# Kernel optimization log

Measured on AMD Instinct MI355X. Metric: run time of the kernel, lower is better.

## Reference

```python
import jax, jax.numpy as jnp
import numpy as np

T, N = 32, 256
HID, NL = 64, 1
D_CH, Hg, Wg = 2, 8, 8            # obs shape (2, 8, 8); d must be 2 to match Conv2d(2*HID, 2*HID)
NSUB, SUBDIM = 6, 3               # subtasks shape (n_subtasks, subtask_dim)
OBS_V, SUB_V, NACT = 16, 20, 6    # vocab sizes; action_space.n = NSUB
OBS_LEN = D_CH * Hg * Wg          # 128
SUB_LEN = NSUB * SUBDIM           # 18
GRU_IN = HID * (OBS_LEN + SUBDIM) # 8384
STATE = 2 + NL * HID + NACT + NSUB  # a(1)+v(1)+h(64)+a_probs(6)+p(6) = 78


def setup_inputs() -> dict:
    key = jax.random.key(0)
    ks = jax.random.split(key, 12)
    obs_idx = jax.random.randint(ks[0], (T, N, OBS_LEN), 0, OBS_V)
    sub_idx = jax.random.randint(ks[1], (T, N, SUB_LEN), 0, SUB_V)
    act = jax.random.randint(ks[2], (T, N, 1), 0, NACT)  # all >= 0 -> sample_new is a no-op
    inputs = jnp.concatenate([obs_idx, sub_idx, act], -1).astype(jnp.float32)
    hx = jnp.zeros((1, N, STATE), jnp.float32)  # all-zero -> new_episode everywhere
    sd = lambda f: 1.0 / np.sqrt(f)
    return dict(
        inputs=inputs,
        hx=hx,
        subtask_emb=jax.random.normal(ks[3], (SUB_V, HID)),
        obs_emb=jax.random.normal(ks[4], (OBS_V, HID)),
        conv_w=jax.random.normal(ks[5], (2 * HID, 2 * HID)) * sd(2 * HID),
        conv_b=jnp.zeros((2 * HID,)),
        w_ih=jax.random.normal(ks[6], (3 * HID, GRU_IN)) * sd(GRU_IN),
        w_hh=jax.random.normal(ks[7], (3 * HID, HID)) * sd(HID),
        b_ih=jnp.zeros((3 * HID,)),
        b_hh=jnp.zeros((3 * HID,)),
        critic_w=jax.random.normal(ks[8], (1, HID)) * sd(HID),
        critic_b=jnp.zeros((1,)),
        phi_w=jax.random.normal(ks[9], (1, HID)) * sd(HID),
        phi_b=jnp.zeros((1,)),
    )


def _forward(inputs, hx, subtask_emb, obs_emb, conv_w, conv_b, w_ih, w_hh,
             b_ih, b_hh, critic_w, critic_b, phi_w, phi_b):
    ints = inputs.astype(jnp.int32)
    obs_all = ints[:, :, :OBS_LEN]                      # (T,N,128)
    sub_all = ints[:, :, OBS_LEN:OBS_LEN + SUB_LEN]     # (T,N,18)
    act_all = ints[:, :, -1]                            # (T,N)

    # subtask memory from first timestep: (N, NSUB, SUBDIM*HID)
    M = subtask_emb[sub_all[0]].reshape(N, NSUB, SUBDIM * HID)

    hx0 = hx[0]
    new_episode = jnp.all(hx0 == 0, axis=-1)            # (N,)
    # recurrent state split order a(1), v(1), h(NL*HID), a_probs(NACT), p(NSUB)
    h0 = hx0[:, 2:2 + NL * HID].reshape(N, NL, HID).transpose(1, 0, 2)  # (NL,N,HID)
    p0 = hx0[:, 2 + NL * HID + NACT:]
    p0 = p0.at[:, 0].set(jnp.where(new_episode, 1.0, p0[:, 0]))

    def gru_cell(x, h):
        gx = x @ w_ih.T + b_ih
        gh = h @ w_hh.T + b_hh
        r = jax.nn.sigmoid(gx[:, :HID] + gh[:, :HID])
        z = jax.nn.sigmoid(gx[:, HID:2 * HID] + gh[:, HID:2 * HID])
        n = jnp.tanh(gx[:, 2 * HID:] + r * gh[:, 2 * HID:])
        return (1 - z) * n + z * h

    def step(carry, xt):
        h, p = carry
        obs_t, act_t = xt
        r_vec = jnp.einsum('ns,nsk->nk', p, M)          # (p.unsqueeze(1) @ M).squeeze(1)
        emb = obs_emb[obs_t.reshape(N, D_CH, Hg, Wg)]   # (N,2,H,W,HID)
        conv_in = emb.transpose(0, 1, 4, 2, 3).reshape(N, 2 * HID, Hg * Wg)
        conv_out = jnp.einsum('ncp,oc->nop', conv_in, conv_w) + conv_b[None, :, None]  # 1x1 conv
        gru_in = jnp.concatenate([conv_out.reshape(N, -1), r_vec], -1)
        hn = gru_cell(gru_in, h[0])                     # single-layer GRU, seq len 1
        h_new = hn[None]
        c = jax.nn.sigmoid(hn @ phi_w.T + phi_b)        # (N,1)
        # torch.roll(F.pad(p,(0,1)), 1) flattened: pad column is 0, so this is a
        # right-shift with 0 fill; p1[:, -1] == p[:, -1].
        p1 = jnp.concatenate([jnp.zeros((N, 1), p.dtype), p[:, :-1]], axis=1)
        p2 = p1 + p * p[:, -1:]
        p_new = (1 - c) * p + c * p2
        probs = p_new / p_new.sum(-1, keepdims=True)    # FixedCategorical(p).probs
        v = hn @ critic_w.T + critic_b                  # (N,1)
        a = act_t.astype(jnp.float32)[:, None]          # actions all >=0 -> no resampling
        h_flat = h_new.transpose(1, 0, 2).reshape(N, -1)
        ys = jnp.concatenate([a, v, h_flat, probs, p_new], -1)
        return (h_new, p_new), ys

    _, hx_out = jax.lax.scan(step, (h0, p0), (obs_all, act_all))  # (T,N,78)
    return hx_out


def reference(inputs, hx, subtask_emb, obs_emb, conv_w, conv_b, w_ih, w_hh,
              b_ih, b_hh, critic_w, critic_b, phi_w, phi_b):
    hx_out = _forward(inputs, hx, subtask_emb, obs_emb, conv_w, conv_b, w_ih,
                      w_hh, b_ih, b_hh, critic_w, critic_b, phi_w, phi_b)
    return (hx_out, hx_out[-1:])
```

## Files before the change

### kernel.cpp

```cpp
#include <hip/hip_runtime.h>
#include <hip/hip_bf16.h>
#include <math.h>

#define TT 32
#define NN 256
#define HID 64
#define OBS_LEN 128
#define SUB_LEN 18
#define IN_ROW 147
#define GJ 192
#define GRU_IN 8384
#define STATE 78
#define NSUB 6

__device__ __forceinline__ float sigm(float x) {
    return 1.0f / (1.0f + __expf(-x));
}

__device__ __forceinline__ unsigned short f2bf(float f) {
    unsigned u = __float_as_uint(f);
    u += 0x7fffu + ((u >> 16) & 1u);
    return (unsigned short)(u >> 16);
}

__global__ void k_T(const float* __restrict__ w_ih, float* __restrict__ wT) {
    __shared__ float tile[32][33];
    int i0 = blockIdx.x * 32;
    int j0 = blockIdx.y * 32;
    int tx = threadIdx.x, ty = threadIdx.y;
    for (int a = ty; a < 32; a += 8)
        tile[a][tx] = w_ih[(size_t)(j0 + a) * GRU_IN + i0 + tx];
    __syncthreads();
    for (int a = ty; a < 32; a += 8)
        wT[(size_t)(i0 + a) * GJ + j0 + tx] = tile[tx][a];
}

__global__ void k_G(const float* __restrict__ obs_emb, const float* __restrict__ conv_w,
                    float* __restrict__ G) {
    int i = blockIdx.x * blockDim.x + threadIdx.x;
    if (i >= 128 * 2 * 16) return;
    int v = i & 15, d = (i >> 4) & 1, o = i >> 5;
    float acc = 0.f;
    const float* oe = obs_emb + v * 64;
    const float* cw = conv_w + o * 128 + d * 64;
    #pragma unroll
    for (int hd = 0; hd < 64; hd++) acc = fmaf(oe[hd], cw[hd], acc);
    G[i] = acc;
}

__global__ void k_CB(const float* __restrict__ conv_b, const float* __restrict__ w_ih,
                     const float* __restrict__ b_ih, float* __restrict__ CB2) {
    int j = blockIdx.x;
    int tid = threadIdx.x;
    const float* wr = w_ih + (size_t)j * GRU_IN;
    float acc = 0.f;
    for (int i = tid; i < 8192; i += 256) acc = fmaf(conv_b[i >> 6], wr[i], acc);
    __shared__ float red[4];
    for (int off = 32; off > 0; off >>= 1) acc += __shfl_down(acc, off, 64);
    if ((tid & 63) == 0) red[tid >> 6] = acc;
    __syncthreads();
    if (tid == 0) CB2[j] = b_ih[j] + red[0] + red[1] + red[2] + red[3];
}

__global__ __launch_bounds__(192) void k_Q(const float* __restrict__ inputs,
                                           const float* __restrict__ subtask_emb,
                                           const float* __restrict__ wT,
                                           float* __restrict__ Q) {
    int n = blockIdx.x;
    int j = threadIdx.x;
    __shared__ int sidx[SUB_LEN];
    __shared__ __align__(16) float Ms[GJ * 8];
    if (j < SUB_LEN) sidx[j] = (int)inputs[(size_t)n * IN_ROW + OBS_LEN + j];
    __syncthreads();
    for (int e = j; e < NSUB * GJ; e += GJ) {
        int s = e / GJ, k = e - s * GJ;
        int row = sidx[s * 3 + (k >> 6)];
        Ms[k * 8 + s] = subtask_emb[row * 64 + (k & 63)];
    }
    __syncthreads();
    float acc[NSUB] = {0.f, 0.f, 0.f, 0.f, 0.f, 0.f};
    const float* base = wT + (size_t)8192 * GJ + j;
    for (int k = 0; k < GJ; k++) {
        float w = base[(size_t)k * GJ];
        float4 m0 = *(const float4*)&Ms[k * 8];
        float2 m1 = *(const float2*)&Ms[k * 8 + 4];
        acc[0] = fmaf(m0.x, w, acc[0]);
        acc[1] = fmaf(m0.y, w, acc[1]);
        acc[2] = fmaf(m0.z, w, acc[2]);
        acc[3] = fmaf(m0.w, w, acc[3]);
        acc[4] = fmaf(m1.x, w, acc[4]);
        acc[5] = fmaf(m1.y, w, acc[5]);
    }
    for (int s = 0; s < NSUB; s++) Q[((size_t)n * NSUB + s) * GJ + j] = acc[s];
}

__global__ __launch_bounds__(192) void k_E(const float* __restrict__ G,
                                           const float* __restrict__ wT,
                                           unsigned short* __restrict__ E16) {
    int bp = blockIdx.x;
    int dp = bp >> 1, half = bp & 1;
    int d = dp >> 6, p = dp & 63;
    int j = threadIdx.x;
    __shared__ __align__(16) float Gs[128 * 8];
    for (int e = j; e < 1024; e += GJ) {
        int o = e >> 3, vv = e & 7;
        Gs[e] = G[(o << 5) + (d << 4) + (half << 3) + vv];
    }
    __syncthreads();
    float acc[8];
    #pragma unroll
    for (int v = 0; v < 8; v++) acc[v] = 0.f;
    const float* wb = wT + (size_t)p * GJ + j;
    for (int o = 0; o < 128; o++) {
        float w = wb[(size_t)(o * 64) * GJ];
        float4 g0 = *(const float4*)&Gs[o * 8];
        float4 g1 = *(const float4*)&Gs[o * 8 + 4];
        acc[0] = fmaf(g0.x, w, acc[0]);
        acc[1] = fmaf(g0.y, w, acc[1]);
        acc[2] = fmaf(g0.z, w, acc[2]);
        acc[3] = fmaf(g0.w, w, acc[3]);
        acc[4] = fmaf(g1.x, w, acc[4]);
        acc[5] = fmaf(g1.y, w, acc[5]);
        acc[6] = fmaf(g1.z, w, acc[6]);
        acc[7] = fmaf(g1.w, w, acc[7]);
    }
    unsigned short* Eo = E16 + ((size_t)(dp * 16 + half * 8)) * GJ;
    #pragma unroll
    for (int v = 0; v < 8; v++) Eo[v * GJ + j] = f2bf(acc[v]);
}

__global__ __launch_bounds__(192) void k_gx(const float* __restrict__ inputs,
                                            const unsigned short* __restrict__ E16,
                                            const float* __restrict__ CB2,
                                            float* __restrict__ gx_all) {
    int tn0 = blockIdx.x * 2;
    int tid = threadIdx.x;
    int g = tid / 96;
    int jj = (tid - g * 96) * 2;
    int tn = tn0 + g;
    __shared__ int idx[2][OBS_LEN];
    for (int e = tid; e < 2 * OBS_LEN; e += 192)
        idx[e >> 7][e & 127] = (int)inputs[(size_t)(tn0 + (e >> 7)) * IN_ROW + (e & 127)];
    __syncthreads();
    float a0 = CB2[jj], a1 = CB2[jj + 1];
    const int* id = idx[g];
    #pragma unroll 8
    for (int dp = 0; dp < OBS_LEN; dp++) {
        unsigned u = *(const unsigned*)(E16 + ((size_t)(dp * 16 + id[dp])) * GJ + jj);
        a0 += __uint_as_float(u << 16);
        a1 += __uint_as_float(u & 0xffff0000u);
    }
    float2 r; r.x = a0; r.y = a1;
    *(float2*)(gx_all + (size_t)tn * GJ + jj) = r;
}

__global__ __launch_bounds__(192) void k_rec(const float* __restrict__ inputs,
                                             const float* __restrict__ hx,
                                             const float* __restrict__ w_hh,
                                             const float* __restrict__ b_hh,
                                             const float* __restrict__ critic_w,
                                             const float* __restrict__ critic_b,
                                             const float* __restrict__ phi_w,
                                             const float* __restrict__ phi_b,
                                             const float* __restrict__ Q,
                                             const float* __restrict__ gx_all,
                                             float* __restrict__ out) {
    int n = blockIdx.x;
    int tid = threadIdx.x;

    __shared__ __align__(16) float gx_lds[TT * GJ];
    __shared__ __align__(16) float h_sh[64];
    __shared__ __align__(16) float p_sh[8];
    __shared__ float sum_sh[GJ];
    __shared__ float ghn_sh[64];
    __shared__ float act_sh[TT];
    __shared__ float sc;
    __shared__ int nz_cnt;

    for (int e = tid * 4; e < TT * GJ; e += 192 * 4) {
        int t = e / GJ, j = e - t * GJ;
        float4 v = *(const float4*)(gx_all + ((size_t)t * NN + n) * GJ + j);
        *(float4*)&gx_lds[e] = v;
    }
    if (tid < TT)
        act_sh[tid] = inputs[((size_t)tid * NN + n) * IN_ROW + (IN_ROW - 1)];

    float wreg[64];
    {
        const float4* wr = (const float4*)(w_hh + (size_t)tid * 64);
        #pragma unroll
        for (int h4 = 0; h4 < 16; h4++) {
            float4 w = wr[h4];
            wreg[h4 * 4 + 0] = w.x;
            wreg[h4 * 4 + 1] = w.y;
            wreg[h4 * 4 + 2] = w.z;
            wreg[h4 * 4 + 3] = w.w;
        }
    }
    float q[NSUB];
    #pragma unroll
    for (int s = 0; s < NSUB; s++) q[s] = Q[((size_t)n * NSUB + s) * GJ + tid];
    float bhh = b_hh[tid];
    float pw = (tid < 64) ? phi_w[tid] : 0.f;
    float cw = (tid < 64) ? critic_w[tid] : 0.f;
    float phib = phi_b[0], crtb = critic_b[0];

    if (tid == 0) nz_cnt = 0;
    __syncthreads();
    if (tid < STATE) {
        float hv = hx[(size_t)n * STATE + tid];
        if (hv != 0.f) atomicAdd(&nz_cnt, 1);
        if (tid >= 2 && tid < 66) h_sh[tid - 2] = hv;
        if (tid >= 72) p_sh[tid - 72] = hv;
    }
    __syncthreads();
    if (tid == 0 && nz_cnt == 0) p_sh[0] = 1.0f;
    __syncthreads();

    for (int t = 0; t < TT; t++) {
        float4 pv = *(const float4*)&p_sh[0];
        float2 pv2 = *(const float2*)&p_sh[4];
        float gx = gx_lds[t * GJ + tid];
        gx = fmaf(pv.x, q[0], gx);
        gx = fmaf(pv.y, q[1], gx);
        gx = fmaf(pv.z, q[2], gx);
        gx = fmaf(pv.w, q[3], gx);
        gx = fmaf(pv2.x, q[4], gx);
        gx = fmaf(pv2.y, q[5], gx);
        float a0 = 0.f, a1 = 0.f, a2 = 0.f, a3 = 0.f;
        #pragma unroll
        for (int h = 0; h < 64; h += 8) {
            float4 ha = *(const float4*)&h_sh[h];
            float4 hb = *(const float4*)&h_sh[h + 4];
            a0 = fmaf(ha.x, wreg[h + 0], a0);
            a1 = fmaf(ha.y, wreg[h + 1], a1);
            a2 = fmaf(ha.z, wreg[h + 2], a2);
            a3 = fmaf(ha.w, wreg[h + 3], a3);
            a0 = fmaf(hb.x, wreg[h + 4], a0);
            a1 = fmaf(hb.y, wreg[h + 5], a1);
            a2 = fmaf(hb.z, wreg[h + 6], a2);
            a3 = fmaf(hb.w, wreg[h + 7], a3);
        }
        float gh = bhh + ((a0 + a1) + (a2 + a3));
        sum_sh[tid] = (tid < 128) ? (gx + gh) : gx;
        if (tid >= 128) ghn_sh[tid - 128] = gh;
        __syncthreads();

        if (tid < 64) {
            float r = sigm(sum_sh[tid]);
            float z = sigm(sum_sh[64 + tid]);
            float x2 = fmaf(r, ghn_sh[tid], sum_sh[128 + tid]);
            float e2 = __expf(2.f * x2);
            float nv = 1.f - 2.f / (e2 + 1.f);
            float hold = h_sh[tid];
            float hn = fmaf(z, hold - nv, nv);
            float pc = hn * pw, vc = hn * cw;
            #pragma unroll
            for (int off = 32; off > 0; off >>= 1) {
                pc += __shfl_down(pc, off, 64);
                vc += __shfl_down(vc, off, 64);
            }
            pc = __shfl(pc, 0, 64);
            float c = sigm(pc + phib);
            if (tid == 0) sc = vc + crtb;
            h_sh[tid] = hn;
            if (tid < NSUB) {
                float pold = p_sh[tid];
                float pm1 = (tid > 0) ? p_sh[tid - 1] : 0.f;
                float p5 = p_sh[5];
                float p2 = pm1 + pold * p5;
                float pn = (1.f - c) * pold + c * p2;
                p_sh[tid] = pn;
            }
        }
        __syncthreads();

        if (tid < STATE) {
            float val;
            if (tid == 0) val = act_sh[t];
            else if (tid == 1) val = sc;
            else if (tid < 66) val = h_sh[tid - 2];
            else if (tid < 72) {
                float ps = p_sh[0] + p_sh[1] + p_sh[2] + p_sh[3] + p_sh[4] + p_sh[5];
                val = p_sh[tid - 66] / ps;
            } else val = p_sh[tid - 72];
            size_t base = ((size_t)t * NN + n) * STATE;
            out[base + tid] = val;
            if (t == TT - 1)
                out[(size_t)TT * NN * STATE + (size_t)n * STATE + tid] = val;
        }
    }
}

extern "C" void kernel_launch(void* const* d_in, const int* in_sizes, int n_in,
                              void* d_out, int out_size, void* d_ws, size_t ws_size,
                              hipStream_t stream) {
    const float* inputs      = (const float*)d_in[0];
    const float* hx          = (const float*)d_in[1];
    const float* subtask_emb = (const float*)d_in[2];
    const float* obs_emb     = (const float*)d_in[3];
    const float* conv_w      = (const float*)d_in[4];
    const float* conv_b      = (const float*)d_in[5];
    const float* w_ih        = (const float*)d_in[6];
    const float* w_hh        = (const float*)d_in[7];
    const float* b_ih        = (const float*)d_in[8];
    const float* b_hh        = (const float*)d_in[9];
    const float* critic_w    = (const float*)d_in[10];
    const float* critic_b    = (const float*)d_in[11];
    const float* phi_w       = (const float*)d_in[12];
    const float* phi_b       = (const float*)d_in[13];
    float* out = (float*)d_out;

    float* ws   = (float*)d_ws;
    float* wT   = ws;
    float* G    = wT + (size_t)GRU_IN * GJ;
    float* CB2  = G + 4096;
    float* Ef   = CB2 + 192;
    unsigned short* E16 = (unsigned short*)Ef;
    float* Q    = Ef + 196608;
    float* gx   = Q + (size_t)NN * NSUB * GJ;

    k_T<<<dim3(GRU_IN / 32, GJ / 32), dim3(32, 8), 0, stream>>>(w_ih, wT);
    k_G<<<16, 256, 0, stream>>>(obs_emb, conv_w, G);
    k_CB<<<GJ, 256, 0, stream>>>(conv_b, w_ih, b_ih, CB2);
    k_Q<<<NN, GJ, 0, stream>>>(inputs, subtask_emb, wT, Q);
    k_E<<<256, GJ, 0, stream>>>(G, wT, E16);
    k_gx<<<TT * NN / 2, GJ, 0, stream>>>(inputs, E16, CB2, gx);
    k_rec<<<NN, GJ, 0, stream>>>(inputs, hx, w_hh, b_hh, critic_w, critic_b,
                                 phi_w, phi_b, Q, gx, out);
}
```

Baseline: 193.7 us.

## Merge setup kernels and run GRU recurrence in a single wavefront per sequence

Three independent preprocessing kernels (weight transpose, conv-embedding table, bias fold) are merged into one launch, and the E and Q precompute kernels into another, cutting launch count from seven to four. The recurrent kernel now uses one 64-lane wavefront per batch element: each lane holds three rows of w_hh in registers and computes all three gates for its hidden unit. This removes the per-step __syncthreads and shared-memory exchange of gate sums, and keeps p in registers with the reductions done by xor shuffles. The trade-off is a much higher register load per lane (192 weight floats) and only 256 single-wave blocks, which lowers occupancy and could cause spills.

```diff
diff --git a/kernel.cpp b/kernel.cpp
--- a/kernel.cpp
+++ b/kernel.cpp
@@ -12,6 +12,7 @@
 #define GRU_IN 8384
 #define STATE 78
 #define NSUB 6
+#define NT_TILES 1572
 
 __device__ __forceinline__ float sigm(float x) {
     return 1.0f / (1.0f + __expf(-x));
@@ -23,110 +24,123 @@
     return (unsigned short)(u >> 16);
 }
 
-__global__ void k_T(const float* __restrict__ w_ih, float* __restrict__ wT) {
+__device__ __forceinline__ float2 pkfma(float2 a, float2 b, float2 c) {
+    float2 r;
+    r.x = fmaf(a.x, b.x, c.x);
+    r.y = fmaf(a.y, b.y, c.y);
+    return r;
+}
+
+__global__ __launch_bounds__(256) void k_TGC(const float* __restrict__ w_ih,
+                                             const float* __restrict__ obs_emb,
+                                             const float* __restrict__ conv_w,
+                                             const float* __restrict__ conv_b,
+                                             const float* __restrict__ b_ih,
+                                             float* __restrict__ wT,
+                                             float* __restrict__ G,
+                                             float* __restrict__ CB2) {
+    int b = blockIdx.x;
+    int tid = threadIdx.x;
     __shared__ float tile[32][33];
-    int i0 = blockIdx.x * 32;
-    int j0 = blockIdx.y * 32;
-    int tx = threadIdx.x, ty = threadIdx.y;
-    for (int a = ty; a < 32; a += 8)
-        tile[a][tx] = w_ih[(size_t)(j0 + a) * GRU_IN + i0 + tx];
-    __syncthreads();
-    for (int a = ty; a < 32; a += 8)
-        wT[(size_t)(i0 + a) * GJ + j0 + tx] = tile[tx][a];
-}
-
-__global__ void k_G(const float* __restrict__ obs_emb, const float* __restrict__ conv_w,
-                    float* __restrict__ G) {
-    int i = blockIdx.x * blockDim.x + threadIdx.x;
-    if (i >= 128 * 2 * 16) return;
-    int v = i & 15, d = (i >> 4) & 1, o = i >> 5;
-    float acc = 0.f;
-    const float* oe = obs_emb + v * 64;
-    const float* cw = conv_w + o * 128 + d * 64;
-    #pragma unroll
-    for (int hd = 0; hd < 64; hd++) acc = fmaf(oe[hd], cw[hd], acc);
-    G[i] = acc;
-}
-
-__global__ void k_CB(const float* __restrict__ conv_b, const float* __restrict__ w_ih,
-                     const float* __restrict__ b_ih, float* __restrict__ CB2) {
-    int j = blockIdx.x;
-    int tid = threadIdx.x;
-    const float* wr = w_ih + (size_t)j * GRU_IN;
-    float acc = 0.f;
-    for (int i = tid; i < 8192; i += 256) acc = fmaf(conv_b[i >> 6], wr[i], acc);
     __shared__ float red[4];
-    for (int off = 32; off > 0; off >>= 1) acc += __shfl_down(acc, off, 64);
-    if ((tid & 63) == 0) red[tid >> 6] = acc;
-    __syncthreads();
-    if (tid == 0) CB2[j] = b_ih[j] + red[0] + red[1] + red[2] + red[3];
-}
-
-__global__ __launch_bounds__(192) void k_Q(const float* __restrict__ inputs,
-                                           const float* __restrict__ subtask_emb,
-                                           const float* __restrict__ wT,
-                                           float* __restrict__ Q) {
-    int n = blockIdx.x;
+
+    if (b < NT_TILES) {
+        int bx = b % 262, by = b / 262;
+        int i0 = bx * 32, j0 = by * 32;
+        int tx = tid & 31, ty = tid >> 5;
+        for (int a = ty; a < 32; a += 8)
+            tile[a][tx] = w_ih[(size_t)(j0 + a) * GRU_IN + i0 + tx];
+        __syncthreads();
+        for (int a = ty; a < 32; a += 8)
+            wT[(size_t)(i0 + a) * GJ + j0 + tx] = tile[tx][a];
+    } else if (b < NT_TILES + 16) {
+        int i = (b - NT_TILES) * 256 + tid;
+        int v = i & 15, d = (i >> 4) & 1, o = i >> 5;
+        float acc = 0.f;
+        const float* oe = obs_emb + v * 64;
+        const float* cw = conv_w + o * 128 + d * 64;
+        #pragma unroll
+        for (int hd = 0; hd < 64; hd++) acc = fmaf(oe[hd], cw[hd], acc);
+        G[i] = acc;
+    } else {
+        int j = b - (NT_TILES + 16);
+        const float* wr = w_ih + (size_t)j * GRU_IN;
+        float acc = 0.f;
+        for (int i = tid; i < 8192; i += 256) acc = fmaf(conv_b[i >> 6], wr[i], acc);
+        for (int off = 32; off > 0; off >>= 1) acc += __shfl_down(acc, off, 64);
+        if ((tid & 63) == 0) red[tid >> 6] = acc;
+        __syncthreads();
+        if (tid == 0) CB2[j] = b_ih[j] + red[0] + red[1] + red[2] + red[3];
+    }
+}
+
+__global__ __launch_bounds__(192) void k_EQ(const float* __restrict__ inputs,
+                                            const float* __restrict__ subtask_emb,
+                                            const float* __restrict__ G,
+                                            const float* __restrict__ wT,
+                                            unsigned short* __restrict__ E16,
+                                            float* __restrict__ Q) {
+    int b = blockIdx.x;
     int j = threadIdx.x;
-    __shared__ int sidx[SUB_LEN];
-    __shared__ __align__(16) float Ms[GJ * 8];
-    if (j < SUB_LEN) sidx[j] = (int)inputs[(size_t)n * IN_ROW + OBS_LEN + j];
-    __syncthreads();
-    for (int e = j; e < NSUB * GJ; e += GJ) {
-        int s = e / GJ, k = e - s * GJ;
-        int row = sidx[s * 3 + (k >> 6)];
-        Ms[k * 8 + s] = subtask_emb[row * 64 + (k & 63)];
-    }
-    __syncthreads();
-    float acc[NSUB] = {0.f, 0.f, 0.f, 0.f, 0.f, 0.f};
-    const float* base = wT + (size_t)8192 * GJ + j;
-    for (int k = 0; k < GJ; k++) {
-        float w = base[(size_t)k * GJ];
-        float4 m0 = *(const float4*)&Ms[k * 8];
-        float2 m1 = *(const float2*)&Ms[k * 8 + 4];
-        acc[0] = fmaf(m0.x, w, acc[0]);
-        acc[1] = fmaf(m0.y, w, acc[1]);
-        acc[2] = fmaf(m0.z, w, acc[2]);
-        acc[3] = fmaf(m0.w, w, acc[3]);
-        acc[4] = fmaf(m1.x, w, acc[4]);
-        acc[5] = fmaf(m1.y, w, acc[5]);
-    }
-    for (int s = 0; s < NSUB; s++) Q[((size_t)n * NSUB + s) * GJ + j] = acc[s];
-}
-
-__global__ __launch_bounds__(192) void k_E(const float* __restrict__ G,
-                                           const float* __restrict__ wT,
-                                           unsigned short* __restrict__ E16) {
-    int bp = blockIdx.x;
-    int dp = bp >> 1, half = bp & 1;
-    int d = dp >> 6, p = dp & 63;
-    int j = threadIdx.x;
-    __shared__ __align__(16) float Gs[128 * 8];
-    for (int e = j; e < 1024; e += GJ) {
-        int o = e >> 3, vv = e & 7;
-        Gs[e] = G[(o << 5) + (d << 4) + (half << 3) + vv];
-    }
-    __syncthreads();
-    float acc[8];
-    #pragma unroll
-    for (int v = 0; v < 8; v++) acc[v] = 0.f;
-    const float* wb = wT + (size_t)p * GJ + j;
-    for (int o = 0; o < 128; o++) {
-        float w = wb[(size_t)(o * 64) * GJ];
-        float4 g0 = *(const float4*)&Gs[o * 8];
-        float4 g1 = *(const float4*)&Gs[o * 8 + 4];
-        acc[0] = fmaf(g0.x, w, acc[0]);
-        acc[1] = fmaf(g0.y, w, acc[1]);
-        acc[2] = fmaf(g0.z, w, acc[2]);
-        acc[3] = fmaf(g0.w, w, acc[3]);
-        acc[4] = fmaf(g1.x, w, acc[4]);
-        acc[5] = fmaf(g1.y, w, acc[5]);
-        acc[6] = fmaf(g1.z, w, acc[6]);
-        acc[7] = fmaf(g1.w, w, acc[7]);
-    }
-    unsigned short* Eo = E16 + ((size_t)(dp * 16 + half * 8)) * GJ;
-    #pragma unroll
-    for (int v = 0; v < 8; v++) Eo[v * GJ + j] = f2bf(acc[v]);
+
+    if (b < 256) {
+        int dp = b >> 1, half = b & 1;
+        int d = dp >> 6, p = dp & 63;
+        __shared__ __align__(16) float Gs[128 * 8];
+        for (int e = j; e < 1024; e += GJ) {
+            int o = e >> 3, vv = e & 7;
+            Gs[e] = G[(o << 5) + (d << 4) + (half << 3) + vv];
+        }
+        __syncthreads();
+        float acc[8];
+        #pragma unroll
+        for (int v = 0; v < 8; v++) acc[v] = 0.f;
+        const float* wb = wT + (size_t)p * GJ + j;
+        #pragma unroll 4
+        for (int o = 0; o < 128; o++) {
+            float w = wb[(size_t)(o * 64) * GJ];
+            float4 g0 = *(const float4*)&Gs[o * 8];
+            float4 g1 = *(const float4*)&Gs[o * 8 + 4];
+            acc[0] = fmaf(g0.x, w, acc[0]);
+            acc[1] = fmaf(g0.y, w, acc[1]);
+            acc[2] = fmaf(g0.z, w, acc[2]);
+            acc[3] = fmaf(g0.w, w, acc[3]);
+            acc[4] = fmaf(g1.x, w, acc[4]);
+            acc[5] = fmaf(g1.y, w, acc[5]);
+            acc[6] = fmaf(g1.z, w, acc[6]);
+            acc[7] = fmaf(g1.w, w, acc[7]);
+        }
+        unsigned short* Eo = E16 + ((size_t)(dp * 16 + half * 8)) * GJ;
+        #pragma unroll
+        for (int v = 0; v < 8; v++) Eo[v * GJ + j] = f2bf(acc[v]);
+    } else {
+        int n = b - 256;
+        __shared__ int sidx[SUB_LEN];
+        __shared__ __align__(16) float Ms[GJ * 8];
+        if (j < SUB_LEN) sidx[j] = (int)inputs[(size_t)n * IN_ROW + OBS_LEN + j];
+        __syncthreads();
+        for (int e = j; e < NSUB * GJ; e += GJ) {
+            int s = e / GJ, k = e - s * GJ;
+            int row = sidx[s * 3 + (k >> 6)];
+            Ms[k * 8 + s] = subtask_emb[row * 64 + (k & 63)];
+        }
+        __syncthreads();
+        float acc[NSUB] = {0.f, 0.f, 0.f, 0.f, 0.f, 0.f};
+        const float* base = wT + (size_t)8192 * GJ + j;
+        #pragma unroll 4
+        for (int k = 0; k < GJ; k++) {
+            float w = base[(size_t)k * GJ];
+            float4 m0 = *(const float4*)&Ms[k * 8];
+            float2 m1 = *(const float2*)&Ms[k * 8 + 4];
+            acc[0] = fmaf(m0.x, w, acc[0]);
+            acc[1] = fmaf(m0.y, w, acc[1]);
+            acc[2] = fmaf(m0.z, w, acc[2]);
+            acc[3] = fmaf(m0.w, w, acc[3]);
+            acc[4] = fmaf(m1.x, w, acc[4]);
+            acc[5] = fmaf(m1.y, w, acc[5]);
+        }
+        for (int s = 0; s < NSUB; s++) Q[((size_t)n * NSUB + s) * GJ + j] = acc[s];
+    }
 }
 
 __global__ __launch_bounds__(192) void k_gx(const float* __restrict__ inputs,
@@ -154,141 +168,140 @@
     *(float2*)(gx_all + (size_t)tn * GJ + jj) = r;
 }
 
-__global__ __launch_bounds__(192) void k_rec(const float* __restrict__ inputs,
-                                             const float* __restrict__ hx,
-                                             const float* __restrict__ w_hh,
-                                             const float* __restrict__ b_hh,
-                                             const float* __restrict__ critic_w,
-                                             const float* __restrict__ critic_b,
-                                             const float* __restrict__ phi_w,
-                                             const float* __restrict__ phi_b,
-                                             const float* __restrict__ Q,
-                                             const float* __restrict__ gx_all,
-                                             float* __restrict__ out) {
+__global__ __launch_bounds__(64, 1) void k_rec(const float* __restrict__ inputs,
+                                               const float* __restrict__ hx,
+                                               const float* __restrict__ w_hh,
+                                               const float* __restrict__ b_hh,
+                                               const float* __restrict__ critic_w,
+                                               const float* __restrict__ critic_b,
+                                               const float* __restrict__ phi_w,
+                                               const float* __restrict__ phi_b,
+                                               const float* __restrict__ Q,
+                                               const float* __restrict__ gx_all,
+                                               float* __restrict__ out) {
     int n = blockIdx.x;
-    int tid = threadIdx.x;
+    int lane = threadIdx.x;
 
     __shared__ __align__(16) float gx_lds[TT * GJ];
     __shared__ __align__(16) float h_sh[64];
-    __shared__ __align__(16) float p_sh[8];
-    __shared__ float sum_sh[GJ];
-    __shared__ float ghn_sh[64];
     __shared__ float act_sh[TT];
-    __shared__ float sc;
-    __shared__ int nz_cnt;
-
-    for (int e = tid * 4; e < TT * GJ; e += 192 * 4) {
+
+    for (int e = lane * 4; e < TT * GJ; e += 64 * 4) {
         int t = e / GJ, j = e - t * GJ;
-        float4 v = *(const float4*)(gx_all + ((size_t)t * NN + n) * GJ + j);
-        *(float4*)&gx_lds[e] = v;
-    }
-    if (tid < TT)
-        act_sh[tid] = inputs[((size_t)tid * NN + n) * IN_ROW + (IN_ROW - 1)];
-
-    float wreg[64];
+        *(float4*)&gx_lds[e] = *(const float4*)(gx_all + ((size_t)t * NN + n) * GJ + j);
+    }
+    if (lane < TT)
+        act_sh[lane] = inputs[((size_t)lane * NN + n) * IN_ROW + (IN_ROW - 1)];
+
+    float2 w0[32], w1[32], w2[32];
     {
-        const float4* wr = (const float4*)(w_hh + (size_t)tid * 64);
+        const float4* r0 = (const float4*)(w_hh + (size_t)lane * 64);
+        const float4* r1 = (const float4*)(w_hh + (size_t)(64 + lane) * 64);
+        const float4* r2 = (const float4*)(w_hh + (size_t)(128 + lane) * 64);
         #pragma unroll
         for (int h4 = 0; h4 < 16; h4++) {
-            float4 w = wr[h4];
-            wreg[h4 * 4 + 0] = w.x;
-            wreg[h4 * 4 + 1] = w.y;
-            wreg[h4 * 4 + 2] = w.z;
-            wreg[h4 * 4 + 3] = w.w;
-        }
-    }
-    float q[NSUB];
+            float4 a = r0[h4]; w0[2*h4] = make_float2(a.x, a.y); w0[2*h4+1] = make_float2(a.z, a.w);
+            float4 c = r1[h4]; w1[2*h4] = make_float2(c.x, c.y); w1[2*h4+1] = make_float2(c.z, c.w);
+            float4 d = r2[h4]; w2[2*h4] = make_float2(d.x, d.y); w2[2*h4+1] = make_float2(d.z, d.w);
+        }
+    }
+    float q0[NSUB], q1[NSUB], q2[NSUB];
     #pragma unroll
-    for (int s = 0; s < NSUB; s++) q[s] = Q[((size_t)n * NSUB + s) * GJ + tid];
-    float bhh = b_hh[tid];
-    float pw = (tid < 64) ? phi_w[tid] : 0.f;
-    float cw = (tid < 64) ? critic_w[tid] : 0.f;
+    for (int s = 0; s < NSUB; s++) {
+        const float* qb = Q + ((size_t)n * NSUB + s) * GJ;
+        q0[s] = qb[lane]; q1[s] = qb[64 + lane]; q2[s] = qb[128 + lane];
+    }
+    float bh0 = b_hh[lane], bh1 = b_hh[64 + lane], bh2 = b_hh[128 + lane];
+    float pw = phi_w[lane], cw = critic_w[lane];
     float phib = phi_b[0], crtb = critic_b[0];
 
-    if (tid == 0) nz_cnt = 0;
-    __syncthreads();
-    if (tid < STATE) {
-        float hv = hx[(size_t)n * STATE + tid];
-        if (hv != 0.f) atomicAdd(&nz_cnt, 1);
-        if (tid >= 2 && tid < 66) h_sh[tid - 2] = hv;
-        if (tid >= 72) p_sh[tid - 72] = hv;
-    }
-    __syncthreads();
-    if (tid == 0 && nz_cnt == 0) p_sh[0] = 1.0f;
-    __syncthreads();
+    float v0 = hx[(size_t)n * STATE + lane];
+    float v1 = (lane < STATE - 64) ? hx[(size_t)n * STATE + 64 + lane] : 0.f;
+    unsigned long long bal0 = __ballot(v0 != 0.f);
+    unsigned long long bal1 = __ballot((lane < STATE - 64) && v1 != 0.f);
+    bool ne = ((bal0 | bal1) == 0ULL);
+    float h_own = hx[(size_t)n * STATE + 2 + lane];
+    float p0, p1, p2, p3, p4, p5;
+    {
+        const float* pb = hx + (size_t)n * STATE + 72;
+        p0 = pb[0]; p1 = pb[1]; p2 = pb[2]; p3 = pb[3]; p4 = pb[4]; p5 = pb[5];
+    }
+    if (ne) p0 = 1.0f;
+    h_sh[lane] = h_own;
 
     for (int t = 0; t < TT; t++) {
-        float4 pv = *(const float4*)&p_sh[0];
-        float2 pv2 = *(const float2*)&p_sh[4];
-        float gx = gx_lds[t * GJ + tid];
-        gx = fmaf(pv.x, q[0], gx);
-        gx = fmaf(pv.y, q[1], gx);
-        gx = fmaf(pv.z, q[2], gx);
-        gx = fmaf(pv.w, q[3], gx);
-        gx = fmaf(pv2.x, q[4], gx);
-        gx = fmaf(pv2.y, q[5], gx);
-        float a0 = 0.f, a1 = 0.f, a2 = 0.f, a3 = 0.f;
-        #pragma unroll
-        for (int h = 0; h < 64; h += 8) {
-            float4 ha = *(const float4*)&h_sh[h];
-            float4 hb = *(const float4*)&h_sh[h + 4];
-            a0 = fmaf(ha.x, wreg[h + 0], a0);
-            a1 = fmaf(ha.y, wreg[h + 1], a1);
-            a2 = fmaf(ha.z, wreg[h + 2], a2);
-            a3 = fmaf(ha.w, wreg[h + 3], a3);
-            a0 = fmaf(hb.x, wreg[h + 4], a0);
-            a1 = fmaf(hb.y, wreg[h + 5], a1);
-            a2 = fmaf(hb.z, wreg[h + 6], a2);
-            a3 = fmaf(hb.w, wreg[h + 7], a3);
-        }
-        float gh = bhh + ((a0 + a1) + (a2 + a3));
-        sum_sh[tid] = (tid < 128) ? (gx + gh) : gx;
-        if (tid >= 128) ghn_sh[tid - 128] = gh;
-        __syncthreads();
-
-        if (tid < 64) {
-            float r = sigm(sum_sh[tid]);
-            float z = sigm(sum_sh[64 + tid]);
-            float x2 = fmaf(r, ghn_sh[tid], sum_sh[128 + tid]);
-            float e2 = __expf(2.f * x2);
-            float nv = 1.f - 2.f / (e2 + 1.f);
-            float hold = h_sh[tid];
-            float hn = fmaf(z, hold - nv, nv);
-            float pc = hn * pw, vc = hn * cw;
-            #pragma unroll
-            for (int off = 32; off > 0; off >>= 1) {
-                pc += __shfl_down(pc, off, 64);
-                vc += __shfl_down(vc, off, 64);
-            }
-            pc = __shfl(pc, 0, 64);
-            float c = sigm(pc + phib);
-            if (tid == 0) sc = vc + crtb;
-            h_sh[tid] = hn;
-            if (tid < NSUB) {
-                float pold = p_sh[tid];
-                float pm1 = (tid > 0) ? p_sh[tid - 1] : 0.f;
-                float p5 = p_sh[5];
-                float p2 = pm1 + pold * p5;
-                float pn = (1.f - c) * pold + c * p2;
-                p_sh[tid] = pn;
-            }
-        }
-        __syncthreads();
-
-        if (tid < STATE) {
-            float val;
-            if (tid == 0) val = act_sh[t];
-            else if (tid == 1) val = sc;
-            else if (tid < 66) val = h_sh[tid - 2];
-            else if (tid < 72) {
-                float ps = p_sh[0] + p_sh[1] + p_sh[2] + p_sh[3] + p_sh[4] + p_sh[5];
-                val = p_sh[tid - 66] / ps;
-            } else val = p_sh[tid - 72];
-            size_t base = ((size_t)t * NN + n) * STATE;
-            out[base + tid] = val;
-            if (t == TT - 1)
-                out[(size_t)TT * NN * STATE + (size_t)n * STATE + tid] = val;
-        }
+        float gx0 = gx_lds[t * GJ + lane];
+        float gx1 = gx_lds[t * GJ + 64 + lane];
+        float gx2 = gx_lds[t * GJ + 128 + lane];
+        gx0 = fmaf(p0, q0[0], gx0); gx1 = fmaf(p0, q1[0], gx1); gx2 = fmaf(p0, q2[0], gx2);
+        gx0 = fmaf(p1, q0[1], gx0); gx1 = fmaf(p1, q1[1], gx1); gx2 = fmaf(p1, q2[1], gx2);
+        gx0 = fmaf(p2, q0[2], gx0); gx1 = fmaf(p2, q1[2], gx1); gx2 = fmaf(p2, q2[2], gx2);
+        gx0 = fmaf(p3, q0[3], gx0); gx1 = fmaf(p3, q1[3], gx1); gx2 = fmaf(p3, q2[3], gx2);
+        gx0 = fmaf(p4, q0[4], gx0); gx1 = fmaf(p4, q1[4], gx1); gx2 = fmaf(p4, q2[4], gx2);
+        gx0 = fmaf(p5, q0[5], gx0); gx1 = fmaf(p5, q1[5], gx1); gx2 = fmaf(p5, q2[5], gx2);
+        float2 a0 = make_float2(0.f, 0.f), a1 = a0, a2 = a0;
+        #pragma unroll
+        for (int h4 = 0; h4 < 16; h4++) {
+            float4 hh = *(const float4*)&h_sh[h4 * 4];
+            float2 hA = make_float2(hh.x, hh.y);
+            float2 hB = make_float2(hh.z, hh.w);
+            a0 = pkfma(hA, w0[2*h4], a0); a0 = pkfma(hB, w0[2*h4+1], a0);
+            a1 = pkfma(hA, w1[2*h4], a1); a1 = pkfma(hB, w1[2*h4+1], a1);
+            a2 = pkfma(hA, w2[2*h4], a2); a2 = pkfma(hB, w2[2*h4+1], a2);
+        }
+        float gh0 = bh0 + a0.x + a0.y;
+        float gh1 = bh1 + a1.x + a1.y;
+        float gh2 = bh2 + a2.x + a2.y;
+
+        float r = sigm(gx0 + gh0);
+        float z = sigm(gx1 + gh1);
+        float x2 = fmaf(r, gh2, gx2);
+        float e2 = __expf(2.f * x2);
+        float nv = 1.f - 2.f / (e2 + 1.f);
+        float hn = fmaf(z, h_own - nv, nv);
+
+        float pc = hn * pw, vc = hn * cw;
+        #pragma unroll
+        for (int off = 32; off > 0; off >>= 1) {
+            pc += __shfl_xor(pc, off, 64);
+            vc += __shfl_xor(vc, off, 64);
+        }
+        float c = sigm(pc + phib);
+        float v = vc + crtb;
+
+        float n0 = fmaf(c, (p0 * p5)      - p0, p0);
+        float n1 = fmaf(c, (p0 + p1 * p5) - p1, p1);
+        float n2 = fmaf(c, (p1 + p2 * p5) - p2, p2);
+        float n3 = fmaf(c, (p2 + p3 * p5) - p3, p3);
+        float n4 = fmaf(c, (p3 + p4 * p5) - p4, p4);
+        float n5 = fmaf(c, (p4 + p5 * p5) - p5, p5);
+        float psum = ((n0 + n1) + (n2 + n3)) + (n4 + n5);
+        float rinv = 1.0f / psum;
+
+        size_t base = ((size_t)t * NN + n) * STATE;
+        out[base + 2 + lane] = hn;
+        int sidx = (lane < 6) ? lane : lane - 6;
+        float ppick = n0;
+        ppick = (sidx == 1) ? n1 : ppick;
+        ppick = (sidx == 2) ? n2 : ppick;
+        ppick = (sidx == 3) ? n3 : ppick;
+        ppick = (sidx == 4) ? n4 : ppick;
+        ppick = (sidx == 5) ? n5 : ppick;
+        if (lane < 12) {
+            out[base + 66 + lane] = (lane < 6) ? ppick * rinv : ppick;
+        } else if (lane < 14) {
+            out[base + (lane - 12)] = (lane == 12) ? act_sh[t] : v;
+        }
+        if (t == TT - 1) {
+            size_t b2 = (size_t)TT * NN * STATE + (size_t)n * STATE;
+            out[b2 + 2 + lane] = hn;
+            if (lane < 12) out[b2 + 66 + lane] = (lane < 6) ? ppick * rinv : ppick;
+            else if (lane < 14) out[b2 + (lane - 12)] = (lane == 12) ? act_sh[t] : v;
+        }
+
+        h_sh[lane] = hn;
+        h_own = hn;
+        p0 = n0; p1 = n1; p2 = n2; p3 = n3; p4 = n4; p5 = n5;
     }
 }
 
@@ -320,12 +333,10 @@
     float* Q    = Ef + 196608;
     float* gx   = Q + (size_t)NN * NSUB * GJ;
 
-    k_T<<<dim3(GRU_IN / 32, GJ / 32), dim3(32, 8), 0, stream>>>(w_ih, wT);
-    k_G<<<16, 256, 0, stream>>>(obs_emb, conv_w, G);
-    k_CB<<<GJ, 256, 0, stream>>>(conv_b, w_ih, b_ih, CB2);
-    k_Q<<<NN, GJ, 0, stream>>>(inputs, subtask_emb, wT, Q);
-    k_E<<<256, GJ, 0, stream>>>(G, wT, E16);
+    k_TGC<<<NT_TILES + 16 + GJ, 256, 0, stream>>>(w_ih, obs_emb, conv_w, conv_b,
+                                                  b_ih, wT, G, CB2);
+    k_EQ<<<512, GJ, 0, stream>>>(inputs, subtask_emb, G, wT, E16, Q);
     k_gx<<<TT * NN / 2, GJ, 0, stream>>>(inputs, E16, CB2, gx);
-    k_rec<<<NN, GJ, 0, stream>>>(inputs, hx, w_hh, b_hh, critic_w, critic_b,
+    k_rec<<<NN, 64, 0, stream>>>(inputs, hx, w_hh, b_hh, critic_w, critic_b,
                                  phi_w, phi_b, Q, gx, out);
 }
```

Measured after the change: 188.9 us. 2.5% less time.
